# Kernel optimization log

Hardware: AMD Instinct MI355X
Metric: run time of the kernel (lower is better)

The kernel has to match this reference:

```python
import jax, jax.numpy as jnp
import numpy as np

B, D, K = 4096, 512, 64


def setup_inputs() -> dict:
    key = jax.random.key(0)
    k1, k2, k3, k4, k5, k6 = jax.random.split(key, 6)
    observations = jax.random.normal(k1, (B, D), dtype=jnp.float32)
    # binary mask (1 = observed, 0 = missing), stored as float for multiply
    mask = jnp.round(jax.random.uniform(k2, (B, D), dtype=jnp.float32))
    F = jax.random.normal(k3, (1, D, 10), dtype=jnp.float32) * 0.1
    b = jax.random.normal(k4, (1, D, 1), dtype=jnp.float32) * 0.1
    W = jax.random.normal(k5, (11, K), dtype=jnp.float32) * 0.1
    bw = jax.random.normal(k6, (K,), dtype=jnp.float32) * 0.1
    return {"observations": observations, "mask": mask, "F": F, "b": b, "W": W, "bw": bw}


def reference(observations, mask, F, b, W, bw):
    # x_aug per (batch, feature): [x*F_d (10), b_d (1)] -> 11-dim
    Bn = observations.shape[0]
    xF = observations[:, :, None] * F[0]                      # [B, D, 10]
    b_bc = jnp.broadcast_to(b[0], (observations.shape[1], 1)) # [D, 1]
    aug = jnp.concatenate([xF, jnp.broadcast_to(b_bc, (Bn,) + b_bc.shape)], axis=-1)  # [B, D, 11]
    encoded = jnp.einsum('bdf,fk->bdk', aug, W) + bw          # [B, D, K]
    out = jax.nn.relu(jnp.sum(encoded * mask[:, :, None], axis=1))  # [B, K]
    return out
```

## Files before the change

kernel.cpp:

```cpp
#include <hip/hip_runtime.h>
#include <hip/hip_bf16.h>


#define D_DIM 512
#define K_DIM 64
#define B_DIM 4096

typedef __attribute__((ext_vector_type(4))) float f32x4;
typedef __attribute__((ext_vector_type(8))) short bf16x8;

__device__ __forceinline__ unsigned short f2bf(float f) {
    unsigned u = __builtin_bit_cast(unsigned, f);
    u += 0x7fffu + ((u >> 16) & 1u);
    return (unsigned short)(u >> 16);
}
__device__ __forceinline__ unsigned pack2(float a, float b) {
    return (unsigned)f2bf(a) | ((unsigned)f2bf(b) << 16);
}

__global__ __launch_bounds__(256, 2)
void fused_kernel(const float* __restrict__ obs,
                  const float* __restrict__ mask,
                  const float* __restrict__ bvec,
                  const float* __restrict__ F,
                  const float* __restrict__ W,
                  const float* __restrict__ bw,
                  float* __restrict__ out) {
    __shared__ __align__(16) unsigned short GF[4096 * 8];
    __shared__ __align__(16) unsigned short XF[512 * 8];
    __shared__ float s0s[8], s1s[8];

    const int tid  = threadIdx.x;
    const int lane = tid & 63;
    const int w    = tid >> 6;
    const int ln   = lane & 15;
    const int g    = lane >> 4;
    const int rowbase = blockIdx.x * 8;

    const int r = tid >> 5;
    const int c = tid & 31;
    const float* orow = obs  + (size_t)(rowbase + r) * D_DIM;
    const float* mrow = mask + (size_t)(rowbase + r) * D_DIM;
    f32x4 o[4], m[4], bv[4];
#pragma unroll
    for (int j = 0; j < 4; ++j) {
        int d = c * 4 + 128 * j;
        o[j]  = *reinterpret_cast<const f32x4*>(orow + d);
        m[j]  = *reinterpret_cast<const f32x4*>(mrow + d);
        bv[j] = *reinterpret_cast<const f32x4*>(bvec + d);
    }

    {
        bf16x8 wf[4];
#pragma unroll
        for (int nt = 0; nt < 4; ++nt) {
#pragma unroll
            for (int j = 0; j < 8; ++j) {
                int k = g * 8 + j;
                wf[nt][j] = (k < 10)
                    ? (short)f2bf(W[k * K_DIM + nt * 16 + ln]) : (short)0;
            }
        }
#pragma unroll
        for (int i = 0; i < 8; ++i) {
            const int dt = w * 8 + i;
            const int Frow = dt * 16 + ln;
            const float* Fr = F + (size_t)Frow * 10;
            float fa[8] = {0.f, 0.f, 0.f, 0.f, 0.f, 0.f, 0.f, 0.f};
            if (g == 0) {
                float2 t0 = *reinterpret_cast<const float2*>(Fr + 0);
                float2 t1 = *reinterpret_cast<const float2*>(Fr + 2);
                float2 t2 = *reinterpret_cast<const float2*>(Fr + 4);
                float2 t3 = *reinterpret_cast<const float2*>(Fr + 6);
                fa[0] = t0.x; fa[1] = t0.y; fa[2] = t1.x; fa[3] = t1.y;
                fa[4] = t2.x; fa[5] = t2.y; fa[6] = t3.x; fa[7] = t3.y;
            } else if (g == 1) {
                float2 t = *reinterpret_cast<const float2*>(Fr + 8);
                fa[0] = t.x; fa[1] = t.y;
            }
            bf16x8 af;
#pragma unroll
            for (int j = 0; j < 8; ++j) af[j] = (short)f2bf(fa[j]);

#pragma unroll
            for (int nt = 0; nt < 4; ++nt) {
                f32x4 gacc = {0.f, 0.f, 0.f, 0.f};
                gacc = __builtin_amdgcn_mfma_f32_16x16x32_bf16(af, wf[nt], gacc, 0, 0, 0);
                int slot = (nt * 16 + (dt >> 1)) * 64 + ((dt & 1) * 2 + (g >> 1)) * 16 + ln;
                uint2 val;
                val.x = pack2(gacc[0], gacc[1]);
                val.y = pack2(gacc[2], gacc[3]);
                *reinterpret_cast<uint2*>(
                    reinterpret_cast<char*>(GF) + slot * 16 + (g & 1) * 8) = val;
            }
        }
    }

    {
        float p0 = 0.f, p1 = 0.f;
#pragma unroll
        for (int j = 0; j < 4; ++j) {
            uint2 xv;
            xv.x = pack2(o[j].x * m[j].x, o[j].y * m[j].y);
            xv.y = pack2(o[j].z * m[j].z, o[j].w * m[j].w);
            int tp   = (c >> 3) + 4 * j;
            int gch  = (c >> 1) & 3;
            int slot = r * 64 + ((tp * 4 + gch) ^ r);
            *reinterpret_cast<uint2*>(
                reinterpret_cast<char*>(XF) + slot * 16 + (c & 1) * 8) = xv;
            p0 += (m[j].x + m[j].y) + (m[j].z + m[j].w);
            p1 = fmaf(m[j].x, bv[j].x, p1);
            p1 = fmaf(m[j].y, bv[j].y, p1);
            p1 = fmaf(m[j].z, bv[j].z, p1);
            p1 = fmaf(m[j].w, bv[j].w, p1);
        }
#pragma unroll
        for (int s = 1; s <= 16; s <<= 1) {
            p0 += __shfl_xor(p0, s, 64);
            p1 += __shfl_xor(p1, s, 64);
        }
        if (c == 0) { s0s[r] = p0; s1s[r] = p1; }
    }
    __syncthreads();

    f32x4 acc = {0.f, 0.f, 0.f, 0.f};
    {
        const int arow = lane & 7;
        const char* xb = reinterpret_cast<const char*>(XF);
        const char* gb = reinterpret_cast<const char*>(GF);
#pragma unroll
        for (int tp = 0; tp < 16; ++tp) {
            bf16x8 a = *reinterpret_cast<const bf16x8*>(
                xb + (arow * 64 + ((tp * 4 + g) ^ arow)) * 16);
            bf16x8 b = *reinterpret_cast<const bf16x8*>(
                gb + ((w * 16 + tp) * 64 + lane) * 16);
            acc = __builtin_amdgcn_mfma_f32_16x16x32_bf16(a, b, acc, 0, 0, 0);
        }
    }

    const int kk = w * 16 + ln;
    if (lane < 32) {
        const float w10 = W[10 * K_DIM + kk];
        const float bwv = bw[kk];
#pragma unroll
        for (int rr = 0; rr < 4; ++rr) {
            const int rowl = g * 4 + rr;
            float tot = acc[rr];
            tot = fmaf(s1s[rowl], w10, tot);
            tot = fmaf(s0s[rowl], bwv, tot);
            out[(size_t)(rowbase + rowl) * K_DIM + kk] = fmaxf(tot, 0.f);
        }
    }
}

extern "C" void kernel_launch(void* const* d_in, const int* in_sizes, int n_in,
                              void* d_out, int out_size, void* d_ws, size_t ws_size,
                              hipStream_t stream) {
    const float* obs  = (const float*)d_in[0];
    const float* mask = (const float*)d_in[1];
    const float* F    = (const float*)d_in[2];
    const float* bvec = (const float*)d_in[3];
    const float* W    = (const float*)d_in[4];
    const float* bw   = (const float*)d_in[5];
    float* out = (float*)d_out;

    fused_kernel<<<B_DIM / 8, 256, 0, stream>>>(obs, mask, bvec, F, W, bw, out);
}
```

Measured before the change: 15.13 us.

## Process two 8-row batches per block with double-buffered staging and prefetch

Each block now handles 16 rows as two 8-row batches. This amortizes the per-block construction of the GF table (F×W product via MFMA) across twice as many rows. The second batch's observation and mask loads are issued before the first batch's MFMA and epilogue, using a double-buffered XF area. The grid is halved to 256 blocks and launch bounds drop to one block per SM, which may cut occupancy and parallelism.

```diff
diff --git a/kernel.cpp b/kernel.cpp
--- a/kernel.cpp
+++ b/kernel.cpp
@@ -18,7 +18,7 @@
     return (unsigned)f2bf(a) | ((unsigned)f2bf(b) << 16);
 }
 
-__global__ __launch_bounds__(256, 2)
+__global__ __launch_bounds__(256, 1)
 void fused_kernel(const float* __restrict__ obs,
                   const float* __restrict__ mask,
                   const float* __restrict__ bvec,
@@ -27,28 +27,36 @@
                   const float* __restrict__ bw,
                   float* __restrict__ out) {
     __shared__ __align__(16) unsigned short GF[4096 * 8];
-    __shared__ __align__(16) unsigned short XF[512 * 8];
-    __shared__ float s0s[8], s1s[8];
+    __shared__ __align__(16) unsigned short XF[2][512 * 8];
+    __shared__ float s0s[2][8], s1s[2][8];
 
     const int tid  = threadIdx.x;
     const int lane = tid & 63;
     const int w    = tid >> 6;
     const int ln   = lane & 15;
     const int g    = lane >> 4;
-    const int rowbase = blockIdx.x * 8;
+    const int rowbase = blockIdx.x * 16;
 
     const int r = tid >> 5;
     const int c = tid & 31;
-    const float* orow = obs  + (size_t)(rowbase + r) * D_DIM;
-    const float* mrow = mask + (size_t)(rowbase + r) * D_DIM;
-    f32x4 o[4], m[4], bv[4];
+
+    f32x4 bv[4];
 #pragma unroll
-    for (int j = 0; j < 4; ++j) {
-        int d = c * 4 + 128 * j;
-        o[j]  = *reinterpret_cast<const f32x4*>(orow + d);
-        m[j]  = *reinterpret_cast<const f32x4*>(mrow + d);
-        bv[j] = *reinterpret_cast<const f32x4*>(bvec + d);
-    }
+    for (int j = 0; j < 4; ++j)
+        bv[j] = *reinterpret_cast<const f32x4*>(bvec + c * 4 + 128 * j);
+
+    f32x4 o[4], m[4];
+    auto issue_loads = [&](int b) {
+        const float* orow = obs  + (size_t)(rowbase + b * 8 + r) * D_DIM;
+        const float* mrow = mask + (size_t)(rowbase + b * 8 + r) * D_DIM;
+#pragma unroll
+        for (int j = 0; j < 4; ++j) {
+            int d = c * 4 + 128 * j;
+            o[j] = *reinterpret_cast<const f32x4*>(orow + d);
+            m[j] = *reinterpret_cast<const f32x4*>(mrow + d);
+        }
+    };
+    issue_loads(0);
 
     {
         bf16x8 wf[4];
@@ -96,8 +104,13 @@
         }
     }
 
-    {
+    const int kk = w * 16 + ln;
+    const float w10 = W[10 * K_DIM + kk];
+    const float bwv = bw[kk];
+
+    auto stage = [&](int b) {
         float p0 = 0.f, p1 = 0.f;
+        char* xb = reinterpret_cast<char*>(XF[b]);
 #pragma unroll
         for (int j = 0; j < 4; ++j) {
             uint2 xv;
@@ -106,8 +119,7 @@
             int tp   = (c >> 3) + 4 * j;
             int gch  = (c >> 1) & 3;
             int slot = r * 64 + ((tp * 4 + gch) ^ r);
-            *reinterpret_cast<uint2*>(
-                reinterpret_cast<char*>(XF) + slot * 16 + (c & 1) * 8) = xv;
+            *reinterpret_cast<uint2*>(xb + slot * 16 + (c & 1) * 8) = xv;
             p0 += (m[j].x + m[j].y) + (m[j].z + m[j].w);
             p1 = fmaf(m[j].x, bv[j].x, p1);
             p1 = fmaf(m[j].y, bv[j].y, p1);
@@ -119,38 +131,49 @@
             p0 += __shfl_xor(p0, s, 64);
             p1 += __shfl_xor(p1, s, 64);
         }
-        if (c == 0) { s0s[r] = p0; s1s[r] = p1; }
-    }
-    __syncthreads();
+        if (c == 0) { s0s[b][r] = p0; s1s[b][r] = p1; }
+    };
 
-    f32x4 acc = {0.f, 0.f, 0.f, 0.f};
-    {
+    f32x4 acc;
+    auto mfma_batch = [&](int b) {
+        acc[0] = acc[1] = acc[2] = acc[3] = 0.f;
         const int arow = lane & 7;
-        const char* xb = reinterpret_cast<const char*>(XF);
+        const char* xb = reinterpret_cast<const char*>(XF[b]);
         const char* gb = reinterpret_cast<const char*>(GF);
 #pragma unroll
         for (int tp = 0; tp < 16; ++tp) {
             bf16x8 a = *reinterpret_cast<const bf16x8*>(
                 xb + (arow * 64 + ((tp * 4 + g) ^ arow)) * 16);
-            bf16x8 b = *reinterpret_cast<const bf16x8*>(
+            bf16x8 bfr = *reinterpret_cast<const bf16x8*>(
                 gb + ((w * 16 + tp) * 64 + lane) * 16);
-            acc = __builtin_amdgcn_mfma_f32_16x16x32_bf16(a, b, acc, 0, 0, 0);
+            acc = __builtin_amdgcn_mfma_f32_16x16x32_bf16(a, bfr, acc, 0, 0, 0);
         }
-    }
+    };
 
-    const int kk = w * 16 + ln;
-    if (lane < 32) {
-        const float w10 = W[10 * K_DIM + kk];
-        const float bwv = bw[kk];
+    auto epilogue = [&](int b) {
+        if (lane < 32) {
 #pragma unroll
-        for (int rr = 0; rr < 4; ++rr) {
-            const int rowl = g * 4 + rr;
-            float tot = acc[rr];
-            tot = fmaf(s1s[rowl], w10, tot);
-            tot = fmaf(s0s[rowl], bwv, tot);
-            out[(size_t)(rowbase + rowl) * K_DIM + kk] = fmaxf(tot, 0.f);
+            for (int rr = 0; rr < 4; ++rr) {
+                const int rowl = g * 4 + rr;
+                float tot = acc[rr];
+                tot = fmaf(s1s[b][rowl], w10, tot);
+                tot = fmaf(s0s[b][rowl], bwv, tot);
+                out[(size_t)(rowbase + b * 8 + rowl) * K_DIM + kk] = fmaxf(tot, 0.f);
+            }
         }
-    }
+    };
+
+    stage(0);
+    __syncthreads();
+
+    issue_loads(1);
+    mfma_batch(0);
+    epilogue(0);
+    stage(1);
+    __syncthreads();
+
+    mfma_batch(1);
+    epilogue(1);
 }
 
 extern "C" void kernel_launch(void* const* d_in, const int* in_sizes, int n_in,
@@ -164,5 +187,5 @@
     const float* bw   = (const float*)d_in[5];
     float* out = (float*)d_out;
 
-    fused_kernel<<<B_DIM / 8, 256, 0, stream>>>(obs, mask, bvec, F, W, bw, out);
+    fused_kernel<<<B_DIM / 16, 256, 0, stream>>>(obs, mask, bvec, F, W, bw, out);
 }
```

Measured after the change: 14.83 us. -2.0%, faster.
